# Kernel tuning notes

Hardware: AMD Instinct MI355X
Metric: run time of the kernel (lower is better)

## Reference

```python
import jax, jax.numpy as jnp
import numpy as np

L, B, H, NI, V = 256, 32, 1024, 1024, 10000


def setup_inputs() -> dict:
    key = jax.random.key(0)
    ks = jax.random.split(key, 8)
    return {
        "input_ids": jax.random.randint(ks[0], (L, B), 0, V),
        "h0": jnp.zeros((B, H), jnp.float32),
        "c0": jnp.zeros((B, H), jnp.float32),
        "emb_w": jax.random.uniform(ks[1], (V, NI), jnp.float32, -0.1, 0.1),
        "w_ih": jax.random.normal(ks[2], (4 * H, NI), jnp.float32) * 0.02,
        "w_hh": jax.random.normal(ks[3], (4 * H, H), jnp.float32) * 0.02,
        "dec_w": jax.random.uniform(ks[4], (V, H), jnp.float32, -0.1, 0.1),
        "dec_b": jnp.zeros((V,), jnp.float32),
        "W": jax.random.normal(ks[5], (H, 1), jnp.float32) * 0.1,
        "U": jax.random.normal(ks[6], (H, 1), jnp.float32) * 0.1,
    }


def reference(input_ids, h0, c0, emb_w, w_ih, w_hh, dec_w, dec_b, W, U):
    seq_len, bsz = input_ids.shape
    nhid = h0.shape[1]
    emb = emb_w[input_ids]  # [L, B, NI]

    def lstm_cell(x, h, c):
        # torch LSTMCell (bias=False), gate order i, f, g, o
        gates = x @ w_ih.T + h @ w_hh.T  # [B, 4H]
        i, f, g, o = jnp.split(gates, 4, axis=-1)
        c_new = jax.nn.sigmoid(f) * c + jax.nn.sigmoid(i) * jnp.tanh(g)
        h_new = jax.nn.sigmoid(o) * jnp.tanh(c_new)
        return h_new, c_new

    time_idx = jnp.arange(seq_len)

    def step(carry, xs):
        h, c, hist = carry  # hist: [L, B, H] padded history of hiddens
        x, i = xs
        h, c = lstm_cell(x, h, c)
        hist = hist.at[i].set(h)
        # additive attention over all hiddens so far
        b = (hist.reshape(-1, nhid) @ U).reshape(seq_len, bsz)  # [L, B]
        a = (h @ W).reshape(1, bsz)  # [1, B]
        scores = jnp.tanh(a + b)
        scores = jnp.where((time_idx <= i)[:, None], scores, -jnp.inf)
        att = jax.nn.softmax(scores, axis=0)  # softmax over time
        ctx = jnp.sum(att[:, :, None] * hist, axis=0)  # [B, H]
        return (h, c, hist), ctx

    hist0 = jnp.zeros((seq_len, bsz, nhid), dtype=h0.dtype)
    (h, c, _), ctx = jax.lax.scan(step, (h0, c0, hist0), (emb, time_idx))
    # ctx: [L, B, H]
    logits = ctx @ dec_w.T + dec_b  # [L, B, V]
    out = jax.nn.log_softmax(logits, axis=-1)
    return out, (h, c)
```

## Files before the change

### kernel.cpp

```cpp
#include <hip/hip_runtime.h>
#include <math.h>

typedef unsigned short u16;
typedef unsigned u32;
typedef unsigned long long u64;
typedef float f32x4 __attribute__((ext_vector_type(4)));
typedef float f32x2 __attribute__((ext_vector_type(2)));
typedef __bf16 bf16x8 __attribute__((ext_vector_type(8)));
typedef u16 u16x8 __attribute__((ext_vector_type(8)));
typedef u16 u16x4 __attribute__((ext_vector_type(4)));
typedef u32 u32x4 __attribute__((ext_vector_type(4)));
typedef u32 u32x2 __attribute__((ext_vector_type(2)));

#define L_SEQ 256
#define BSZ 32
#define HID 1024
#define NIN 1024
#define VOC 10000
#define G4 4096
#define MROWS 8192
#define NB 64
#define NW 160
#define DPB 16
#define SENT 0xFFFFFFFFu
#define NT_N 79

__device__ __forceinline__ u16 f2bf(float f) {
    unsigned u = __float_as_uint(f);
    unsigned r = u + 0x7FFFu + ((u >> 16) & 1u);
    return (u16)(r >> 16);
}
#define BF2F(x) __builtin_bit_cast(float, (u32)((u16)(x)) << 16)

__device__ __forceinline__ float fast_sigm(float x) {
    x = fminf(fmaxf(x, -15.f), 15.f);
    return __builtin_amdgcn_rcpf(1.f + __expf(-x));
}
__device__ __forceinline__ float fast_tanh(float x) {
    x = fminf(fmaxf(x, -15.f), 15.f);
    float t = __expf(2.f * x);
    return (t - 1.f) * __builtin_amdgcn_rcpf(t + 1.f);
}
__device__ __forceinline__ unsigned umax4(u16x8 v) {
    u32x4 c = __builtin_bit_cast(u32x4, v);
    unsigned a = c.x > c.y ? c.x : c.y;
    unsigned b = c.z > c.w ? c.z : c.w;
    return a > b ? a : b;
}

typedef __attribute__((address_space(1))) const unsigned GA;
typedef __attribute__((address_space(3))) unsigned LA;
__device__ __forceinline__ void gload_lds16(const void* g, void* l) {
    __builtin_amdgcn_global_load_lds((GA*)g, (LA*)l, 16, 0, 0);
}

__global__ __launch_bounds__(256) void cvt_bf16_kernel(const float* __restrict__ in,
                                                       u16* __restrict__ out, int n4) {
    int idx = blockIdx.x * 256 + threadIdx.x;
    if (idx < n4) {
        f32x4 v = *(const f32x4*)(in + (size_t)idx * 4);
        u16x4 o = {f2bf(v.x), f2bf(v.y), f2bf(v.z), f2bf(v.w)};
        *(u16x4*)(out + (size_t)idx * 4) = o;
    }
}

__global__ __launch_bounds__(256) void gather_emb_kernel(const int* __restrict__ ids,
                                                         const float* __restrict__ emb_w,
                                                         u16* __restrict__ out) {
    int m = blockIdx.x;
    int id = ids[m];
    const float* src = emb_w + (size_t)id * NIN;
    u16* dst = out + (size_t)m * NIN;
    int t = threadIdx.x;
    f32x4 v = *(const f32x4*)(src + t * 4);
    u16x4 o = {f2bf(v.x), f2bf(v.y), f2bf(v.z), f2bf(v.w)};
    *(u16x4*)(dst + t * 4) = o;
}

__global__ __launch_bounds__(256) void gemm_dec_kernel(const u16* __restrict__ A,
                                                       const u16* __restrict__ B,
                                                       float* __restrict__ C,
                                                       const float* __restrict__ bias) {
    __shared__ alignas(16) u16 Asl[128 * 32];
    __shared__ alignas(16) u16 Bsl[128 * 32];
    int bid = blockIdx.x;
    int swz = (bid & 7) * ((NT_N * 64) >> 3) + (bid >> 3);
    int nt = swz >> 6;
    int mt = swz & 63;
    int m0 = mt * 128, n0 = nt * 128;

    int t = threadIdx.x;
    int lane = t & 63, w = t >> 6;
    int wr = w >> 1, wc = w & 1;
    int l15 = lane & 15, l4 = lane >> 4;
    int rsub = lane >> 2;
    int kof = (lane & 3) * 8;

    f32x4 acc[4][4];
    f32x4 zv = {0.f, 0.f, 0.f, 0.f};
    for (int mi = 0; mi < 4; ++mi)
        for (int ni = 0; ni < 4; ++ni) acc[mi][ni] = zv;

    for (int k0 = 0; k0 < HID; k0 += 32) {
#pragma unroll
        for (int s = 0; s < 2; ++s) {
            int row = s * 64 + w * 16 + rsub;
            const u16* gA = A + (size_t)(m0 + row) * HID + k0 + kof;
            gload_lds16(gA, Asl + (s * 64 + w * 16) * 32);
            int brow = n0 + row;
            if (brow > VOC - 1) brow = VOC - 1;
            const u16* gB = B + (size_t)brow * HID + k0 + kof;
            gload_lds16(gB, Bsl + (s * 64 + w * 16) * 32);
        }
        __syncthreads();
        bf16x8 af[4], bfr[4];
        for (int mi = 0; mi < 4; ++mi)
            af[mi] = __builtin_bit_cast(bf16x8,
                                        *(const u16x8*)(Asl + (wr * 64 + mi * 16 + l15) * 32 + l4 * 8));
        for (int ni = 0; ni < 4; ++ni)
            bfr[ni] = __builtin_bit_cast(bf16x8,
                                         *(const u16x8*)(Bsl + (wc * 64 + ni * 16 + l15) * 32 + l4 * 8));
        for (int mi = 0; mi < 4; ++mi)
            for (int ni = 0; ni < 4; ++ni)
                acc[mi][ni] = __builtin_amdgcn_mfma_f32_16x16x32_bf16(af[mi], bfr[ni], acc[mi][ni], 0, 0, 0);
        __syncthreads();
    }

    for (int mi = 0; mi < 4; ++mi)
        for (int ni = 0; ni < 4; ++ni) {
            int col = n0 + wc * 64 + ni * 16 + l15;
            if (col < VOC) {
                float bb = bias[col];
                int rbase = m0 + wr * 64 + mi * 16 + l4 * 4;
                for (int r = 0; r < 4; ++r)
                    C[(size_t)(rbase + r) * VOC + col] = acc[mi][ni][r] + bb;
            }
        }
}

__global__ __launch_bounds__(256, 1) void lstm_seq_kernel(
    const float* __restrict__ c0, const u16* __restrict__ w_hh_bf, u16* __restrict__ gxT,
    const float* __restrict__ Wv, const float* __restrict__ Uv, u16* __restrict__ hb_hist,
    float* __restrict__ out_tail, float* __restrict__ part_ab, const u16* __restrict__ A_emb,
    const u16* __restrict__ w_ih_bf) {
    __shared__ alignas(16) u16 Bs[64][1024];
    __shared__ float gsm[4][32][17];
    __shared__ float c_sl[32][17];

    int blk = blockIdx.x;
    int t = threadIdx.x;
    int lane = t & 63, wave = t >> 6;
    int l15 = lane & 15, l4 = lane >> 4;

    if (blk >= NB) {
        u16(*As2)[40] = (u16(*)[40])(&Bs[0][0]);
        u16(*Bs2)[40] = (u16(*)[40])((char*)(&Bs[0][0]) + 10240);
        int wr = wave >> 1, wc = wave & 1;
        for (int tau = blk - NB; tau < 2048; tau += NW) {
            int m0 = (tau >> 5) * 128;
            int n0 = (tau & 31) * 128;
            f32x4 acc[4][4];
            f32x4 zv = {0.f, 0.f, 0.f, 0.f};
            for (int mi = 0; mi < 4; ++mi)
                for (int ni = 0; ni < 4; ++ni) acc[mi][ni] = zv;
            for (int k0 = 0; k0 < NIN; k0 += 32) {
                for (int s = 0; s < 2; ++s) {
                    int task = t + s * 256;
                    int row = task >> 2, kof = (task & 3) * 8;
                    *(u16x8*)(&As2[row][kof]) =
                        *(const u16x8*)(A_emb + (size_t)(m0 + row) * NIN + k0 + kof);
                    *(u16x8*)(&Bs2[row][kof]) =
                        *(const u16x8*)(w_ih_bf + (size_t)(n0 + row) * NIN + k0 + kof);
                }
                __syncthreads();
                bf16x8 af[4], bfr[4];
                for (int mi = 0; mi < 4; ++mi)
                    af[mi] = __builtin_bit_cast(bf16x8,
                                                *(const u16x8*)(&As2[wr * 64 + mi * 16 + l15][l4 * 8]));
                for (int ni = 0; ni < 4; ++ni)
                    bfr[ni] = __builtin_bit_cast(bf16x8,
                                                 *(const u16x8*)(&Bs2[wc * 64 + ni * 16 + l15][l4 * 8]));
                for (int mi = 0; mi < 4; ++mi)
                    for (int ni = 0; ni < 4; ++ni)
                        acc[mi][ni] =
                            __builtin_amdgcn_mfma_f32_16x16x32_bf16(af[mi], bfr[ni], acc[mi][ni], 0, 0, 0);
                __syncthreads();
            }
            for (int mi = 0; mi < 4; ++mi)
                for (int ni = 0; ni < 4; ++ni) {
                    int n = n0 + wc * 64 + ni * 16 + l15;
                    int g = n >> 10, dd = n & 1023;
                    int dblk = dd >> 4, dl = dd & 15;
                    int mbase = m0 + wr * 64 + mi * 16 + l4 * 4;
                    int i = mbase >> 5, bb2 = mbase & 31;
                    size_t idx = ((((size_t)dblk * L_SEQ + i) * 4 + g) * 16 + dl) * 32 + bb2;
                    u32 lo = (u32)f2bf(acc[mi][ni][0]) | ((u32)f2bf(acc[mi][ni][1]) << 16);
                    u32 hi = (u32)f2bf(acc[mi][ni][2]) | ((u32)f2bf(acc[mi][ni][3]) << 16);
                    u64 pk = (u64)lo | ((u64)hi << 32);
                    __hip_atomic_store((u64*)(gxT + idx), pk, __ATOMIC_RELAXED,
                                       __HIP_MEMORY_SCOPE_AGENT);
                }
        }
        return;
    }

    int d0 = blk * DPB;
    int wm = wave & 1, wn = wave >> 1;

    for (int s = 0; s < 32; ++s) {
        int cid = t + s * 256;
        int c = cid >> 7;
        int ch = cid & 127;
        int g = c >> 4, dl = c & 15;
        u16x8 v = *(const u16x8*)(w_hh_bf + (size_t)(g * HID + d0 + dl) * HID + ch * 8);
        int chs = ch ^ (c & 7);
        *(u16x8*)(&Bs[c][chs * 8]) = v;
    }
    for (int s = t; s < 512; s += 256) {
        int b = s >> 4, dl = s & 15;
        c_sl[b][dl] = c0[b * HID + d0 + dl];
    }
    __syncthreads();

    int cA = wn * 32 + l15;
    int cB = cA + 16;
    int sw = cA & 7;
    int gA = cA >> 4, dA = cA & 15;
    int gB = cB >> 4, dB = cB & 15;

    int bb = t >> 3;
    int pr = t & 7;
    int dl0 = pr * 2;

    const u16* gxTb = gxT + (size_t)blk * ((size_t)L_SEQ * 2048) + wm * 16 + l4 * 4;

    u16x4 gw0, gw1;
    {
        const u16* p0 = gxTb + gA * 512 + dA * 32;
        const u16* p1 = gxTb + gB * 512 + dB * 32;
        asm volatile("global_load_dwordx2 %0, %1, off sc0 sc1" : "=v"(gw0) : "v"(p0));
        asm volatile("global_load_dwordx2 %0, %1, off sc0 sc1" : "=v"(gw1) : "v"(p1));
    }

    for (int i = 0; i < L_SEQ; ++i) {
        const u16* hb = hb_hist + (size_t)i * (BSZ * HID);
        const u16* aptr = hb + (size_t)(wm * 16 + l15) * HID + l4 * 8;
        const u16* cp0 = gxTb + (size_t)i * 2048 + gA * 512 + dA * 32;
        const u16* cp1 = gxTb + (size_t)i * 2048 + gB * 512 + dB * 32;

        u16x8 afr[32];
#pragma unroll
        for (int kk = 0; kk < 32; ++kk)
            asm volatile("global_load_dwordx4 %0, %1, off offset:%c2 sc0 sc1"
                         : "=v"(afr[kk])
                         : "v"(aptr), "n"(kk * 64));

        f32x4 acc0 = {0.f, 0.f, 0.f, 0.f}, acc1 = {0.f, 0.f, 0.f, 0.f};
        unsigned pend = 0xFFFFFFFFu;
        for (;;) {
            asm volatile("s_waitcnt vmcnt(0)" ::: "memory");
            __builtin_amdgcn_sched_barrier(0);
            unsigned done = 0;
#pragma unroll
            for (int kk = 0; kk < 32; ++kk) {
                if (pend & (1u << kk)) {
                    if (__ballot(umax4(afr[kk]) == SENT) == 0) {
                        bf16x8 af = __builtin_bit_cast(bf16x8, afr[kk]);
                        int ch = kk * 4 + l4;
                        bf16x8 b0 = __builtin_bit_cast(bf16x8, *(const u16x8*)(&Bs[cA][(ch ^ sw) * 8]));
                        bf16x8 b1 = __builtin_bit_cast(bf16x8, *(const u16x8*)(&Bs[cB][(ch ^ sw) * 8]));
                        acc0 = __builtin_amdgcn_mfma_f32_16x16x32_bf16(af, b0, acc0, 0, 0, 0);
                        acc1 = __builtin_amdgcn_mfma_f32_16x16x32_bf16(af, b1, acc1, 0, 0, 0);
                        done |= 1u << kk;
                    }
                }
            }
            pend &= ~done;
            if (!pend) break;
#pragma unroll
            for (int kk = 0; kk < 32; ++kk)
                if (pend & (1u << kk))
                    asm volatile("global_load_dwordx4 %0, %1, off offset:%c2 sc0 sc1"
                                 : "=v"(afr[kk])
                                 : "v"(aptr), "n"(kk * 64));
            __builtin_amdgcn_s_sleep(1);
        }
        __builtin_amdgcn_sched_barrier(0);

        for (;;) {
            u32x2 w0 = __builtin_bit_cast(u32x2, gw0);
            u32x2 w1 = __builtin_bit_cast(u32x2, gw1);
            if (__ballot(w0.x == SENT || w0.y == SENT || w1.x == SENT || w1.y == SENT) == 0) break;
            __builtin_amdgcn_s_sleep(4);
            asm volatile("global_load_dwordx2 %0, %1, off sc0 sc1" : "=v"(gw0) : "v"(cp0));
            asm volatile("global_load_dwordx2 %0, %1, off sc0 sc1" : "=v"(gw1) : "v"(cp1));
            asm volatile("s_waitcnt vmcnt(0)" ::: "memory");
            __builtin_amdgcn_sched_barrier(0);
        }

#pragma unroll
        for (int r = 0; r < 4; ++r) {
            int m = wm * 16 + l4 * 4 + r;
            gsm[gA][m][dA] = acc0[r] + BF2F(gw0[r]);
            gsm[gB][m][dB] = acc1[r] + BF2F(gw1[r]);
        }
        __syncthreads();

        u16* hb_next = hb_hist + (size_t)(i + 1) * (BSZ * HID);
        float hn01[2];
#pragma unroll
        for (int q = 0; q < 2; ++q) {
            int dl = dl0 + q;
            float ig = gsm[0][bb][dl], fg = gsm[1][bb][dl];
            float gg = gsm[2][bb][dl], og = gsm[3][bb][dl];
            float cn = fast_sigm(fg) * c_sl[bb][dl] + fast_sigm(ig) * fast_tanh(gg);
            float hn = fast_sigm(og) * fast_tanh(cn);
            c_sl[bb][dl] = cn;
            hn01[q] = hn;
        }
        unsigned pk = (unsigned)f2bf(hn01[0]) | ((unsigned)f2bf(hn01[1]) << 16);
        __hip_atomic_store((unsigned*)(hb_next + bb * HID + d0 + dl0), pk,
                           __ATOMIC_RELAXED, __HIP_MEMORY_SCOPE_AGENT);
        if (i == L_SEQ - 1) {
            f32x2 hv = {hn01[0], hn01[1]};
            *(f32x2*)(out_tail + (size_t)bb * HID + d0 + dl0) = hv;
        }
        float pa = hn01[0] * Wv[d0 + dl0] + hn01[1] * Wv[d0 + dl0 + 1];
        float pb = hn01[0] * Uv[d0 + dl0] + hn01[1] * Uv[d0 + dl0 + 1];
        pa += __shfl_xor(pa, 1); pb += __shfl_xor(pb, 1);
        pa += __shfl_xor(pa, 2); pb += __shfl_xor(pb, 2);
        pa += __shfl_xor(pa, 4); pb += __shfl_xor(pb, 4);
        if (pr == 0) {
            f32x2 pv = {pa, pb};
            *(f32x2*)(part_ab + (((size_t)i * NB + blk) * BSZ + bb) * 2) = pv;
        }

        {
            int inx = (i + 1 < L_SEQ) ? i + 1 : i;
            const u16* np0 = gxTb + (size_t)inx * 2048 + gA * 512 + dA * 32;
            const u16* np1 = gxTb + (size_t)inx * 2048 + gB * 512 + dB * 32;
            asm volatile("global_load_dwordx2 %0, %1, off sc0 sc1" : "=v"(gw0) : "v"(np0));
            asm volatile("global_load_dwordx2 %0, %1, off sc0 sc1" : "=v"(gw1) : "v"(np1));
        }
    }

    for (int s = t; s < 512; s += 256) {
        int b2 = s >> 4, dl = s & 15;
        out_tail[(size_t)BSZ * HID + b2 * HID + d0 + dl] = c_sl[b2][dl];
    }
}

__global__ __launch_bounds__(256) void reduce_ab_kernel(const float* __restrict__ part_ab,
                                                        float* __restrict__ a_arr,
                                                        float* __restrict__ b_arr) {
    int i = blockIdx.x;
    int t = threadIdx.x;
    int b = t & 31, q = t >> 5;
    float sa = 0.f, sb = 0.f;
    for (int j = 0; j < 8; ++j) {
        int blk = q * 8 + j;
        f32x2 v = *(const f32x2*)(part_ab + (((size_t)i * NB + blk) * BSZ + b) * 2);
        sa += v.x;
        sb += v.y;
    }
    __shared__ float ra[8][32], rb[8][32];
    ra[q][b] = sa;
    rb[q][b] = sb;
    __syncthreads();
    if (q == 0) {
        for (int j = 1; j < 8; ++j) { sa += ra[j][b]; sb += rb[j][b]; }
        a_arr[i * BSZ + b] = sa;
        b_arr[i * BSZ + b] = sb;
    }
}

__global__ __launch_bounds__(256) void attn_kernel(const float* __restrict__ a_arr,
                                                   const float* __restrict__ b_arr,
                                                   const u16* __restrict__ hb_hist,
                                                   u16* __restrict__ ctx_bf) {
    int b = blockIdx.y;
    int i0 = blockIdx.x * 8;
    int t = threadIdx.x;
    __shared__ float att[8][256];
    __shared__ float red[256];

    float bt = b_arr[t * BSZ + b];
    for (int q = 0; q < 8; ++q) {
        int iq = i0 + q;
        att[q][t] = (t <= iq) ? tanhf(a_arr[iq * BSZ + b] + bt) : -INFINITY;
    }
    __syncthreads();
    for (int q = 0; q < 8; ++q) {
        int iq = i0 + q;
        red[t] = att[q][t];
        __syncthreads();
        for (int s = 128; s > 0; s >>= 1) {
            if (t < s) red[t] = fmaxf(red[t], red[t + s]);
            __syncthreads();
        }
        float m = red[0];
        __syncthreads();
        float e = (t <= iq) ? expf(att[q][t] - m) : 0.f;
        red[t] = e;
        __syncthreads();
        for (int s = 128; s > 0; s >>= 1) {
            if (t < s) red[t] += red[t + s];
            __syncthreads();
        }
        float sum = red[0];
        __syncthreads();
        att[q][t] = e / sum;
        __syncthreads();
    }

    int hc = t * 4;
    f32x4 accq[8];
    f32x4 zv = {0.f, 0.f, 0.f, 0.f};
    for (int q = 0; q < 8; ++q) accq[q] = zv;
    int imax = i0 + 7;
    for (int t2 = 0; t2 <= imax; ++t2) {
        u16x4 hq = *(const u16x4*)(hb_hist + (size_t)(t2 + 1) * (BSZ * HID) + (size_t)b * HID + hc);
        f32x4 hv = {BF2F(hq.x), BF2F(hq.y), BF2F(hq.z), BF2F(hq.w)};
        for (int q = 0; q < 8; ++q) accq[q] += hv * att[q][t2];
    }
    for (int q = 0; q < 8; ++q) {
        size_t row = (size_t)(i0 + q) * BSZ + b;
        u16x4 o = {f2bf(accq[q].x), f2bf(accq[q].y), f2bf(accq[q].z), f2bf(accq[q].w)};
        *(u16x4*)(ctx_bf + row * HID + hc) = o;
    }
}

__global__ __launch_bounds__(256) void logsoftmax_kernel(float* __restrict__ x, int V) {
    int row = blockIdx.x;
    float* p = x + (size_t)row * V;
    __shared__ float red[256];
    int t = threadIdx.x;
    float frag[40];
    float m = -INFINITY;
#pragma unroll
    for (int k = 0; k < 40; ++k) {
        int j = t + k * 256;
        if (j < VOC) {
            frag[k] = p[j];
            m = fmaxf(m, frag[k]);
        }
    }
    red[t] = m;
    __syncthreads();
    for (int s = 128; s > 0; s >>= 1) {
        if (t < s) red[t] = fmaxf(red[t], red[t + s]);
        __syncthreads();
    }
    m = red[0];
    __syncthreads();
    float sum = 0.f;
#pragma unroll
    for (int k = 0; k < 40; ++k) {
        int j = t + k * 256;
        if (j < VOC) sum += __expf(frag[k] - m);
    }
    red[t] = sum;
    __syncthreads();
    for (int s = 128; s > 0; s >>= 1) {
        if (t < s) red[t] += red[t + s];
        __syncthreads();
    }
    float lse = m + logf(red[0]);
#pragma unroll
    for (int k = 0; k < 40; ++k) {
        int j = t + k * 256;
        if (j < VOC) p[j] = frag[k] - lse;
    }
}

extern "C" void kernel_launch(void* const* d_in, const int* in_sizes, int n_in,
                              void* d_out, int out_size, void* d_ws, size_t ws_size,
                              hipStream_t stream) {
    const int* ids = (const int*)d_in[0];
    const float* h0 = (const float*)d_in[1];
    const float* c0 = (const float*)d_in[2];
    const float* emb_w = (const float*)d_in[3];
    const float* w_ih = (const float*)d_in[4];
    const float* w_hh = (const float*)d_in[5];
    const float* dec_w = (const float*)d_in[6];
    const float* dec_b = (const float*)d_in[7];
    const float* Wv = (const float*)d_in[8];
    const float* Uv = (const float*)d_in[9];

    char* p = (char*)d_ws;
    auto alloc = [&](size_t bytes) {
        void* r = (void*)p;
        p += (bytes + 255) & ~(size_t)255;
        return r;
    };
    u16* w_ih_bf = (u16*)alloc((size_t)G4 * NIN * 2);
    u16* w_hh_bf = (u16*)alloc((size_t)G4 * HID * 2);
    u16* dec_w_bf = (u16*)alloc((size_t)VOC * HID * 2);
    u16* hb_hist = (u16*)alloc((size_t)(L_SEQ + 1) * BSZ * HID * 2);
    u16* A_emb = (u16*)alloc((size_t)MROWS * NIN * 2);
    u16* ctx_bf = (u16*)alloc((size_t)MROWS * HID * 2);
    float* part_ab = (float*)alloc((size_t)L_SEQ * NB * BSZ * 2 * 4);
    float* a_arr = (float*)alloc((size_t)L_SEQ * BSZ * 4);
    float* b_arr = (float*)alloc((size_t)L_SEQ * BSZ * 4);

    float* out = (float*)d_out;
    u16* gxT = (u16*)d_out;
    float* out_tail = out + (size_t)MROWS * VOC;

    cvt_bf16_kernel<<<G4 * NIN / 1024, 256, 0, stream>>>(w_ih, w_ih_bf, G4 * NIN / 4);
    cvt_bf16_kernel<<<G4 * HID / 1024, 256, 0, stream>>>(w_hh, w_hh_bf, G4 * HID / 4);
    cvt_bf16_kernel<<<(VOC * HID / 4 + 255) / 256, 256, 0, stream>>>(dec_w, dec_w_bf, VOC * HID / 4);
    gather_emb_kernel<<<MROWS, 256, 0, stream>>>(ids, emb_w, A_emb);

    hipMemsetAsync(gxT, 0xFF, (size_t)MROWS * G4 * 2, stream);
    hipMemsetAsync(hb_hist + (size_t)BSZ * HID, 0xFF, (size_t)L_SEQ * BSZ * HID * 2, stream);
    cvt_bf16_kernel<<<BSZ * HID / 1024, 256, 0, stream>>>(h0, hb_hist, BSZ * HID / 4);

    lstm_seq_kernel<<<dim3(NB + NW), dim3(256), 0, stream>>>(c0, w_hh_bf, gxT, Wv, Uv, hb_hist,
                                                             out_tail, part_ab, A_emb, w_ih_bf);

    reduce_ab_kernel<<<L_SEQ, 256, 0, stream>>>(part_ab, a_arr, b_arr);
    attn_kernel<<<dim3(L_SEQ / 8, BSZ), 256, 0, stream>>>(a_arr, b_arr, hb_hist, ctx_bf);
    gemm_dec_kernel<<<dim3(64 * NT_N), 256, 0, stream>>>(ctx_bf, dec_w_bf, out, dec_b);
    logsoftmax_kernel<<<MROWS, 256, 0, stream>>>(out, VOC);
}
```

Baseline: 2.447 ms.

## Fuse weight conversions, reswizzle decoder GEMM, enlarge attention query tile

Merges the three fp32-to-bf16 weight conversion launches into a single kernel. Changes the decoder GEMM block-to-tile mapping so that each XCD owns a group of M tiles while sweeping along N, aiming for better L2 reuse. Doubles the attention kernel's query tile to 16 so each history load is reused across more queries, and switches to a fast exp. The larger tile adds register pressure and halves the attention grid size.

```diff
diff --git a/kernel.cpp b/kernel.cpp
--- a/kernel.cpp
+++ b/kernel.cpp
@@ -25,6 +25,10 @@
 #define SENT 0xFFFFFFFFu
 #define NT_N 79
 
+#define NC1 (G4 * NIN / 4)
+#define NC2 (G4 * HID / 4)
+#define NC3 (VOC * HID / 4)
+
 __device__ __forceinline__ u16 f2bf(float f) {
     unsigned u = __float_as_uint(f);
     unsigned r = u + 0x7FFFu + ((u >> 16) & 1u);
@@ -54,14 +58,32 @@
     __builtin_amdgcn_global_load_lds((GA*)g, (LA*)l, 16, 0, 0);
 }
 
+__device__ __forceinline__ void cvt4(const float* in, u16* out, int idx) {
+    f32x4 v = *(const f32x4*)(in + (size_t)idx * 4);
+    u16x4 o = {f2bf(v.x), f2bf(v.y), f2bf(v.z), f2bf(v.w)};
+    *(u16x4*)(out + (size_t)idx * 4) = o;
+}
+
+__global__ __launch_bounds__(256) void cvt_all_kernel(const float* __restrict__ w_ih,
+                                                      u16* __restrict__ w_ih_bf,
+                                                      const float* __restrict__ w_hh,
+                                                      u16* __restrict__ w_hh_bf,
+                                                      const float* __restrict__ dec_w,
+                                                      u16* __restrict__ dec_w_bf) {
+    int idx = blockIdx.x * 256 + threadIdx.x;
+    if (idx < NC1) {
+        cvt4(w_ih, w_ih_bf, idx);
+    } else if (idx < NC1 + NC2) {
+        cvt4(w_hh, w_hh_bf, idx - NC1);
+    } else if (idx < NC1 + NC2 + NC3) {
+        cvt4(dec_w, dec_w_bf, idx - NC1 - NC2);
+    }
+}
+
 __global__ __launch_bounds__(256) void cvt_bf16_kernel(const float* __restrict__ in,
                                                        u16* __restrict__ out, int n4) {
     int idx = blockIdx.x * 256 + threadIdx.x;
-    if (idx < n4) {
-        f32x4 v = *(const f32x4*)(in + (size_t)idx * 4);
-        u16x4 o = {f2bf(v.x), f2bf(v.y), f2bf(v.z), f2bf(v.w)};
-        *(u16x4*)(out + (size_t)idx * 4) = o;
-    }
+    if (idx < n4) cvt4(in, out, idx);
 }
 
 __global__ __launch_bounds__(256) void gather_emb_kernel(const int* __restrict__ ids,
@@ -84,9 +106,10 @@
     __shared__ alignas(16) u16 Asl[128 * 32];
     __shared__ alignas(16) u16 Bsl[128 * 32];
     int bid = blockIdx.x;
-    int swz = (bid & 7) * ((NT_N * 64) >> 3) + (bid >> 3);
-    int nt = swz >> 6;
-    int mt = swz & 63;
+    int xcd = bid & 7;
+    int k = bid >> 3;
+    int mt = (xcd << 3) | (k & 7);
+    int nt = k >> 3;
     int m0 = mt * 128, n0 = nt * 128;
 
     int t = threadIdx.x;
@@ -379,18 +402,18 @@
                                                    const u16* __restrict__ hb_hist,
                                                    u16* __restrict__ ctx_bf) {
     int b = blockIdx.y;
-    int i0 = blockIdx.x * 8;
+    int i0 = blockIdx.x * 16;
     int t = threadIdx.x;
-    __shared__ float att[8][256];
+    __shared__ float att[16][256];
     __shared__ float red[256];
 
     float bt = b_arr[t * BSZ + b];
-    for (int q = 0; q < 8; ++q) {
+    for (int q = 0; q < 16; ++q) {
         int iq = i0 + q;
         att[q][t] = (t <= iq) ? tanhf(a_arr[iq * BSZ + b] + bt) : -INFINITY;
     }
     __syncthreads();
-    for (int q = 0; q < 8; ++q) {
+    for (int q = 0; q < 16; ++q) {
         int iq = i0 + q;
         red[t] = att[q][t];
         __syncthreads();
@@ -400,7 +423,7 @@
         }
         float m = red[0];
         __syncthreads();
-        float e = (t <= iq) ? expf(att[q][t] - m) : 0.f;
+        float e = (t <= iq) ? __expf(att[q][t] - m) : 0.f;
         red[t] = e;
         __syncthreads();
         for (int s = 128; s > 0; s >>= 1) {
@@ -414,16 +437,16 @@
     }
 
     int hc = t * 4;
-    f32x4 accq[8];
+    f32x4 accq[16];
     f32x4 zv = {0.f, 0.f, 0.f, 0.f};
-    for (int q = 0; q < 8; ++q) accq[q] = zv;
-    int imax = i0 + 7;
+    for (int q = 0; q < 16; ++q) accq[q] = zv;
+    int imax = i0 + 15;
     for (int t2 = 0; t2 <= imax; ++t2) {
         u16x4 hq = *(const u16x4*)(hb_hist + (size_t)(t2 + 1) * (BSZ * HID) + (size_t)b * HID + hc);
         f32x4 hv = {BF2F(hq.x), BF2F(hq.y), BF2F(hq.z), BF2F(hq.w)};
-        for (int q = 0; q < 8; ++q) accq[q] += hv * att[q][t2];
-    }
-    for (int q = 0; q < 8; ++q) {
+        for (int q = 0; q < 16; ++q) accq[q] += hv * att[q][t2];
+    }
+    for (int q = 0; q < 16; ++q) {
         size_t row = (size_t)(i0 + q) * BSZ + b;
         u16x4 o = {f2bf(accq[q].x), f2bf(accq[q].y), f2bf(accq[q].z), f2bf(accq[q].w)};
         *(u16x4*)(ctx_bf + row * HID + hc) = o;
@@ -507,9 +530,8 @@
     u16* gxT = (u16*)d_out;
     float* out_tail = out + (size_t)MROWS * VOC;
 
-    cvt_bf16_kernel<<<G4 * NIN / 1024, 256, 0, stream>>>(w_ih, w_ih_bf, G4 * NIN / 4);
-    cvt_bf16_kernel<<<G4 * HID / 1024, 256, 0, stream>>>(w_hh, w_hh_bf, G4 * HID / 4);
-    cvt_bf16_kernel<<<(VOC * HID / 4 + 255) / 256, 256, 0, stream>>>(dec_w, dec_w_bf, VOC * HID / 4);
+    cvt_all_kernel<<<(NC1 + NC2 + NC3 + 255) / 256, 256, 0, stream>>>(w_ih, w_ih_bf, w_hh,
+                                                                      w_hh_bf, dec_w, dec_w_bf);
     gather_emb_kernel<<<MROWS, 256, 0, stream>>>(ids, emb_w, A_emb);
 
     hipMemsetAsync(gxT, 0xFF, (size_t)MROWS * G4 * 2, stream);
@@ -520,7 +542,7 @@
                                                              out_tail, part_ab, A_emb, w_ih_bf);
 
     reduce_ab_kernel<<<L_SEQ, 256, 0, stream>>>(part_ab, a_arr, b_arr);
-    attn_kernel<<<dim3(L_SEQ / 8, BSZ), 256, 0, stream>>>(a_arr, b_arr, hb_hist, ctx_bf);
+    attn_kernel<<<dim3(L_SEQ / 16, BSZ), 256, 0, stream>>>(a_arr, b_arr, hb_hist, ctx_bf);
     gemm_dec_kernel<<<dim3(64 * NT_N), 256, 0, stream>>>(ctx_bf, dec_w_bf, out, dec_b);
     logsoftmax_kernel<<<MROWS, 256, 0, stream>>>(out, VOC);
 }
```

Result: no change. 2.444 ms (median of 2 runs) (-0.2%).
